# Kernel tuning notes

Measured on AMD Instinct MI355X. Metric: run time of the kernel, lower is better.

Reference implementation:

```python
import jax, jax.numpy as jnp
import numpy as np

B, N, C_IN, C_OUT, BASIS = 8, 128, 64, 64, 15
AVG_NOBJ = 49.0
NEG_SLOPE = 0.01  # torch LeakyReLU default


def eops_2_to_2_sum(x, average_nobj=AVG_NOBJ):
    """x: [B, C, N, N] -> [B, C, 15, N, N].
    5 order-zero ops + 10 sum-aggregation ops (sums normalized by average_nobj,
    double sums by average_nobj**2, as in PELICAN's 'sum' aggregation)."""
    n = x.shape[-1]
    eye = jnp.eye(n, dtype=x.dtype)                       # [N, N]
    d = jnp.diagonal(x, axis1=-2, axis2=-1)               # [B, C, N]
    rowsum = x.sum(-1) / average_nobj                      # [B, C, N]
    colsum = x.sum(-2) / average_nobj                      # [B, C, N]
    trace = d.sum(-1) / average_nobj                       # [B, C]
    allsum = x.sum((-2, -1)) / (average_nobj ** 2)         # [B, C]
    bc = lambda v: jnp.broadcast_to(v, x.shape)
    ops = [
        # --- order zero (no aggregation) ---
        d[..., :, None] * eye,                 # diag(A) embedded on diagonal
        bc(d[..., :, None]),                   # A_ii broadcast along j
        bc(d[..., None, :]),                   # A_jj broadcast along i
        x,                                     # identity
        jnp.swapaxes(x, -1, -2),               # transpose
        # --- aggregation ops ---
        rowsum[..., :, None] * eye,            # row sums on diagonal
        colsum[..., :, None] * eye,            # col sums on diagonal
        trace[..., None, None] * eye,          # trace on diagonal
        allsum[..., None, None] * eye,         # total sum on diagonal
        bc(rowsum[..., :, None]),              # rowsum_i broadcast along j
        bc(rowsum[..., None, :]),              # rowsum_j broadcast along i
        bc(colsum[..., :, None]),              # colsum_i broadcast along j
        bc(colsum[..., None, :]),              # colsum_j broadcast along i
        bc(trace[..., None, None]),            # trace broadcast everywhere
        bc(allsum[..., None, None]),           # total sum broadcast everywhere
    ]
    return jnp.stack(ops, axis=2)              # [B, C, 15, N, N]


def setup_inputs() -> dict:
    key = jax.random.key(0)
    ks = jax.random.split(key, 5)
    inputs = jax.random.normal(ks[0], (B, N, N, C_IN), jnp.float32)
    mask = jnp.ones((B, N, N, 1), jnp.float32)
    nobj = jnp.full((B,), float(N), jnp.float32)
    s_b = float(np.sqrt(1.0 / BASIS))
    s_d = float(np.sqrt(1.0 / C_IN))
    coefs00 = jax.random.normal(ks[1], (C_IN, BASIS), jnp.float32) * s_b
    coefs01 = jax.random.normal(ks[2], (C_OUT, BASIS), jnp.float32) * s_b
    coefs10 = jax.random.normal(ks[3], (C_IN, C_OUT), jnp.float32) * s_d
    coefs11 = jax.random.normal(ks[4], (C_IN, C_OUT), jnp.float32) * s_d
    bias = jnp.zeros((C_OUT,), jnp.float32)
    diag_bias = jnp.zeros((C_OUT,), jnp.float32)
    return {"inputs": inputs, "mask": mask, "nobj": nobj,
            "coefs00": coefs00, "coefs01": coefs01,
            "coefs10": coefs10, "coefs11": coefs11,
            "bias": bias, "diag_bias": diag_bias}


def reference(inputs, mask, nobj, coefs00, coefs01, coefs10, coefs11, bias, diag_bias):
    # inputs: [B, N, N, C_in] -> channels-first for basis construction
    x = jnp.transpose(inputs, (0, 3, 1, 2))                     # [B, C, N, N]
    ops = eops_2_to_2_sum(x)                                    # [B, C, 15, N, N]
    # low-rank reconstructed coefficient tensor [C_in, C_out, 15]
    coefs = (coefs00[:, None, :] * coefs10[:, :, None]
             + coefs01[None, :, :] * coefs11[:, :, None])
    out = jnp.einsum('dsb,ndbij->nijs', coefs, ops)             # [B, N, N, C_out]
    eye = jnp.eye(inputs.shape[1], dtype=out.dtype)[None, :, :, None]
    out = out + bias[None, None, None, :] + eye * diag_bias[None, None, None, :]
    out = jax.nn.leaky_relu(out, NEG_SLOPE)
    return out * mask
```

## Files before the change

### kernel.cpp

```cpp
#include <hip/hip_runtime.h>

#define BB 8
#define NN 128
#define CC 64
static constexpr float INV_A = 1.0f / 49.0f;

#define OFF_C    0
#define OFF_CB   61440
#define OFF_RS   65536
#define OFF_CS   131072
#define OFF_DV   196608
#define OFF_TR   262144
#define OFF_AS   262656
#define OFF_U1   263168
#define OFF_U2   328704
#define OFF_DG   394240

typedef __attribute__((ext_vector_type(8))) short v8s;
typedef __attribute__((ext_vector_type(4))) float v4f;

static __device__ inline unsigned pack2bf(float a, float b) {
    union { float f; unsigned u; } ua, ub; ua.f = a; ub.f = b;
    return ((ua.u + 0x8000u) >> 16) | ((ub.u + 0x8000u) & 0xffff0000u);
}
static __device__ inline unsigned short f2bf(float a) {
    union { float f; unsigned u; } ua; ua.f = a;
    return (unsigned short)((ua.u + 0x8000u) >> 16);
}

__global__ void k_coefs(const float* __restrict__ c00, const float* __restrict__ c01,
                        const float* __restrict__ c10, const float* __restrict__ c11,
                        float* __restrict__ ws) {
    int idx = blockIdx.x * 256 + threadIdx.x;
    if (idx < 15 * 4096) {
        int b = idx >> 12; int r = idx & 4095; int d = r >> 6; int s = r & 63;
        ws[OFF_C + idx] = c00[d * 15 + b] * c10[d * 64 + s] + c01[s * 15 + b] * c11[d * 64 + s];
    } else if (idx < 15 * 4096 + 8192) {
        int k = idx - 15 * 4096;
        int which = k >> 12;
        int r = k & 4095; int s = r >> 6; int d = r & 63;
        int b = 3 + which;
        float v = c00[d * 15 + b] * c10[d * 64 + s] + c01[s * 15 + b] * c11[d * 64 + s];
        unsigned short* cb = (unsigned short*)(ws + OFF_CB);
        cb[s * 128 + which * 64 + d] = f2bf(v);
    }
}

__global__ void k_reduce(const float* __restrict__ in, float* __restrict__ ws) {
    __shared__ float4 part[4][4][16];
    int mode = blockIdx.x >> 8;
    int bb = blockIdx.x & 255;
    int n = bb >> 5; int g0 = (bb & 31) * 4;
    int t = threadIdx.x;
    int q = t >> 6; int ii = (t >> 4) & 3; int d4 = t & 15;
    float4 acc = make_float4(0.f, 0.f, 0.f, 0.f);
    if (mode == 0) {
        int i = g0 + ii;
        float4 dvv = acc; bool hd = false;
        const float* base = in + ((size_t)(n * NN + i)) * NN * CC + d4 * 4;
        for (int j = q * 32; j < q * 32 + 32; ++j) {
            float4 v = *(const float4*)(base + (size_t)j * CC);
            acc.x += v.x; acc.y += v.y; acc.z += v.z; acc.w += v.w;
            if (j == i) { dvv = v; hd = true; }
        }
        if (hd) *(float4*)(ws + OFF_DV + ((size_t)(n * NN + i)) * CC + d4 * 4) = dvv;
    } else {
        int j = g0 + ii;
        for (int i = q * 32; i < q * 32 + 32; ++i) {
            float4 v = *(const float4*)(in + (((size_t)(n * NN + i)) * NN + j) * CC + d4 * 4);
            acc.x += v.x; acc.y += v.y; acc.z += v.z; acc.w += v.w;
        }
    }
    part[q][ii][d4] = acc;
    __syncthreads();
    if (t < 64) {
        int i2 = t >> 4; int dd = t & 15;
        float4 a = part[0][i2][dd], b = part[1][i2][dd], c = part[2][i2][dd], d = part[3][i2][dd];
        float4 s;
        s.x = (a.x + b.x + c.x + d.x) * INV_A;
        s.y = (a.y + b.y + c.y + d.y) * INV_A;
        s.z = (a.z + b.z + c.z + d.z) * INV_A;
        s.w = (a.w + b.w + c.w + d.w) * INV_A;
        *(float4*)(ws + (mode ? OFF_CS : OFF_RS) + ((size_t)(n * NN + g0 + i2)) * CC + dd * 4) = s;
    }
}

__global__ void k_traces(float* __restrict__ ws) {
    __shared__ float pt[4][64], pa[4][64];
    int n = blockIdx.x; int t = threadIdx.x;
    int d = t & 63; int q = t >> 6;
    float tr = 0.f, as = 0.f;
    for (int e = 0; e < 32; ++e) {
        int i = q * 32 + e;
        tr += ws[OFF_DV + ((size_t)(n * NN + i)) * CC + d];
        as += ws[OFF_RS + ((size_t)(n * NN + i)) * CC + d];
    }
    pt[q][d] = tr; pa[q][d] = as;
    __syncthreads();
    if (t < 64) {
        float T = pt[0][t] + pt[1][t] + pt[2][t] + pt[3][t];
        float A2 = pa[0][t] + pa[1][t] + pa[2][t] + pa[3][t];
        ws[OFF_TR + n * CC + t] = T * INV_A;
        ws[OFF_AS + n * CC + t] = A2 * INV_A;
    }
}

__global__ void k_uv(const float* __restrict__ bias, const float* __restrict__ dbias,
                     float* __restrict__ ws) {
    int n = blockIdx.x >> 5; int i0 = (blockIdx.x & 31) * 4; int s = threadIdx.x;
    const float* C = ws + OFF_C;
    float aU1[4] = {0, 0, 0, 0}, aU2[4] = {0, 0, 0, 0}, aDG[4] = {0, 0, 0, 0};
    float aS = 0.f, aDGc = 0.f;
    for (int dc = 0; dc < 16; ++dc) {
        float tr4[4], as4[4], dv4[4][4], rs4[4][4], cs4[4][4];
        {
            float4 v = *(const float4*)(ws + OFF_TR + n * CC + dc * 4);
            tr4[0] = v.x; tr4[1] = v.y; tr4[2] = v.z; tr4[3] = v.w;
            float4 w = *(const float4*)(ws + OFF_AS + n * CC + dc * 4);
            as4[0] = w.x; as4[1] = w.y; as4[2] = w.z; as4[3] = w.w;
        }
        #pragma unroll
        for (int ii = 0; ii < 4; ++ii) {
            size_t ro = ((size_t)(n * NN + i0 + ii)) * CC + dc * 4;
            float4 v = *(const float4*)(ws + OFF_DV + ro);
            dv4[ii][0] = v.x; dv4[ii][1] = v.y; dv4[ii][2] = v.z; dv4[ii][3] = v.w;
            float4 r = *(const float4*)(ws + OFF_RS + ro);
            rs4[ii][0] = r.x; rs4[ii][1] = r.y; rs4[ii][2] = r.z; rs4[ii][3] = r.w;
            float4 c = *(const float4*)(ws + OFF_CS + ro);
            cs4[ii][0] = c.x; cs4[ii][1] = c.y; cs4[ii][2] = c.z; cs4[ii][3] = c.w;
        }
        #pragma unroll
        for (int k = 0; k < 4; ++k) {
            int d = dc * 4 + k;
            const float* Cd = C + d * 64 + s;
            float c0 = Cd[0 * 4096], c1 = Cd[1 * 4096], c2 = Cd[2 * 4096];
            float c5 = Cd[5 * 4096], c6 = Cd[6 * 4096], c7 = Cd[7 * 4096];
            float c8 = Cd[8 * 4096], c9 = Cd[9 * 4096], c10v = Cd[10 * 4096];
            float c11v = Cd[11 * 4096], c12v = Cd[12 * 4096];
            float c13 = Cd[13 * 4096], c14 = Cd[14 * 4096];
            aS += c13 * tr4[k] + c14 * as4[k];
            aDGc += c7 * tr4[k] + c8 * as4[k];
            #pragma unroll
            for (int ii = 0; ii < 4; ++ii) {
                aU1[ii] += c1 * dv4[ii][k] + c9 * rs4[ii][k] + c11v * cs4[ii][k];
                aU2[ii] += c2 * dv4[ii][k] + c10v * rs4[ii][k] + c12v * cs4[ii][k];
                aDG[ii] += c0 * dv4[ii][k] + c5 * rs4[ii][k] + c6 * cs4[ii][k];
            }
        }
    }
    float bs = bias[s], dbs = dbias[s];
    for (int ii = 0; ii < 4; ++ii) {
        size_t row = ((size_t)(n * NN + i0 + ii)) * CC + s;
        ws[OFF_U1 + row] = aU1[ii] + aS + bs;
        ws[OFF_U2 + row] = aU2[ii];
        ws[OFF_DG + row] = aDG[ii] + aDGc + dbs;
    }
}

__global__ __launch_bounds__(256, 4) void k_main(
        const float* __restrict__ in, const float* __restrict__ mask,
        const float* __restrict__ ws, float* __restrict__ out) {
    __shared__ __align__(16) unsigned char smem[34816 + 17408];
    unsigned short* Ab = (unsigned short*)smem;
    unsigned short* Bb = (unsigned short*)(smem + 17408);
    float* Obuf = (float*)smem;

    int blk = blockIdx.x;
    int n = blk >> 8; int rem = blk & 255; int i = rem >> 1; int j0 = (rem & 1) * 64;
    int t = threadIdx.x;
    int tp = t >> 4; int c = t & 15;

    const unsigned short* cb = (const unsigned short*)(ws + OFF_CB);
    {
        int cc8 = t & 15;
        #pragma unroll
        for (int e = 0; e < 4; ++e) {
            int s = e * 16 + tp;
            float4 v = *(const float4*)(cb + s * 128 + cc8 * 8);
            *(float4*)((unsigned char*)(Bb + s * 136 + cc8 * 8)) = v;
        }
    }
    {
        const float* src = in + (((size_t)(n * NN + i)) * NN + j0) * CC;
        #pragma unroll
        for (int e = 0; e < 4; ++e) {
            int p = e * 16 + tp;
            float4 v = *(const float4*)(src + (size_t)p * CC + c * 4);
            uint2 pk; pk.x = pack2bf(v.x, v.y); pk.y = pack2bf(v.z, v.w);
            *(uint2*)(Ab + p * 136 + c * 4) = pk;
        }
    }
    {
        #pragma unroll
        for (int e = 0; e < 4; ++e) {
            int p = e * 16 + tp;
            const float* src = in + (((size_t)(n * NN + (j0 + p))) * NN + i) * CC;
            float4 v = *(const float4*)(src + c * 4);
            uint2 pk; pk.x = pack2bf(v.x, v.y); pk.y = pack2bf(v.z, v.w);
            *(uint2*)(Ab + p * 136 + 64 + c * 4) = pk;
        }
    }
    __syncthreads();

    int w = t >> 6; int l = t & 63;
    int r16 = l & 15; int quad = l >> 4;
    v4f acc[4];
    #pragma unroll
    for (int st = 0; st < 4; ++st) acc[st] = 0.f;
    int arow = w * 16 + r16;
    #pragma unroll
    for (int kk = 0; kk < 4; ++kk) {
        v8s af = *(const v8s*)(Ab + arow * 136 + kk * 32 + quad * 8);
        #pragma unroll
        for (int st = 0; st < 4; ++st) {
            v8s bfr = *(const v8s*)(Bb + (st * 16 + r16) * 136 + kk * 32 + quad * 8);
            acc[st] = __builtin_amdgcn_mfma_f32_16x16x32_bf16(af, bfr, acc[st], 0, 0, 0);
        }
    }
    #pragma unroll
    for (int st = 0; st < 4; ++st)
        #pragma unroll
        for (int reg = 0; reg < 4; ++reg)
            Obuf[(w * 16 + quad * 4 + reg) * 68 + st * 16 + r16] = acc[st][reg];
    __syncthreads();

    int srow = (n * NN + i) * CC;
    float4 u1 = *(const float4*)(ws + OFF_U1 + srow + c * 4);
    float4 dg = *(const float4*)(ws + OFF_DG + srow + c * 4);
    #pragma unroll
    for (int e = 0; e < 4; ++e) {
        int p = e * 16 + tp;
        int j = j0 + p;
        float4 v = *(const float4*)(Obuf + p * 68 + c * 4);
        float4 u2 = *(const float4*)(ws + OFF_U2 + (n * NN + j) * CC + c * 4);
        v.x += u1.x + u2.x; v.y += u1.y + u2.y; v.z += u1.z + u2.z; v.w += u1.w + u2.w;
        if (j == i) { v.x += dg.x; v.y += dg.y; v.z += dg.z; v.w += dg.w; }
        v.x = v.x > 0.f ? v.x : 0.01f * v.x;
        v.y = v.y > 0.f ? v.y : 0.01f * v.y;
        v.z = v.z > 0.f ? v.z : 0.01f * v.z;
        v.w = v.w > 0.f ? v.w : 0.01f * v.w;
        float m = mask[((size_t)(n * NN + i)) * NN + j];
        v.x *= m; v.y *= m; v.z *= m; v.w *= m;
        *(float4*)(out + (((size_t)(n * NN + i)) * NN + j) * CC + c * 4) = v;
    }
}

extern "C" void kernel_launch(void* const* d_in, const int* in_sizes, int n_in,
                              void* d_out, int out_size, void* d_ws, size_t ws_size,
                              hipStream_t stream) {
    const float* inputs = (const float*)d_in[0];
    const float* mask   = (const float*)d_in[1];
    const float* c00 = (const float*)d_in[3];
    const float* c01 = (const float*)d_in[4];
    const float* c10 = (const float*)d_in[5];
    const float* c11 = (const float*)d_in[6];
    const float* bias  = (const float*)d_in[7];
    const float* dbias = (const float*)d_in[8];
    float* out = (float*)d_out;
    float* ws = (float*)d_ws;

    k_coefs <<<272, 256, 0, stream>>>(c00, c01, c10, c11, ws);
    k_reduce<<<512, 256, 0, stream>>>(inputs, ws);
    k_traces<<<8, 256, 0, stream>>>(ws);
    k_uv    <<<256, 64, 0, stream>>>(bias, dbias, ws);
    k_main  <<<2048, 256, 0, stream>>>(inputs, mask, ws, out);
}
```

Measured before the change: 151.0 us.

## Merge preprocessing kernels and split k_uv channel reduction across four waves

Folds the coefficient-building kernel into the reduction kernel as extra blocks, and folds the trace/allsum computation into k_uv, so five launches become three. k_uv now runs 256 threads per block, each wave covering a quarter of the input channels, with partial sums combined through shared memory. This is meant to cut launch overhead and the long serial channel loop in the low-occupancy k_uv. The cost is that every k_uv block recomputes the per-batch traces, and the extra shared memory and barriers add some overhead. k_main's shared buffer is also trimmed to the size it actually uses, which may allow more resident blocks.

```diff
diff --git a/kernel.cpp b/kernel.cpp
--- a/kernel.cpp
+++ b/kernel.cpp
@@ -10,8 +10,6 @@
 #define OFF_RS   65536
 #define OFF_CS   131072
 #define OFF_DV   196608
-#define OFF_TR   262144
-#define OFF_AS   262656
 #define OFF_U1   263168
 #define OFF_U2   328704
 #define OFF_DG   394240
@@ -28,25 +26,26 @@
     return (unsigned short)((ua.u + 0x8000u) >> 16);
 }
 
-__global__ void k_coefs(const float* __restrict__ c00, const float* __restrict__ c01,
-                        const float* __restrict__ c10, const float* __restrict__ c11,
-                        float* __restrict__ ws) {
-    int idx = blockIdx.x * 256 + threadIdx.x;
-    if (idx < 15 * 4096) {
-        int b = idx >> 12; int r = idx & 4095; int d = r >> 6; int s = r & 63;
-        ws[OFF_C + idx] = c00[d * 15 + b] * c10[d * 64 + s] + c01[s * 15 + b] * c11[d * 64 + s];
-    } else if (idx < 15 * 4096 + 8192) {
-        int k = idx - 15 * 4096;
-        int which = k >> 12;
-        int r = k & 4095; int s = r >> 6; int d = r & 63;
-        int b = 3 + which;
-        float v = c00[d * 15 + b] * c10[d * 64 + s] + c01[s * 15 + b] * c11[d * 64 + s];
-        unsigned short* cb = (unsigned short*)(ws + OFF_CB);
-        cb[s * 128 + which * 64 + d] = f2bf(v);
-    }
-}
-
-__global__ void k_reduce(const float* __restrict__ in, float* __restrict__ ws) {
+__global__ void k_pre(const float* __restrict__ in,
+                      const float* __restrict__ c00, const float* __restrict__ c01,
+                      const float* __restrict__ c10, const float* __restrict__ c11,
+                      float* __restrict__ ws) {
+    if (blockIdx.x >= 512) {
+        int idx = (blockIdx.x - 512) * 256 + threadIdx.x;
+        if (idx < 15 * 4096) {
+            int b = idx >> 12; int r = idx & 4095; int d = r >> 6; int s = r & 63;
+            ws[OFF_C + idx] = c00[d * 15 + b] * c10[d * 64 + s] + c01[s * 15 + b] * c11[d * 64 + s];
+        } else if (idx < 15 * 4096 + 8192) {
+            int k = idx - 15 * 4096;
+            int which = k >> 12;
+            int r = k & 4095; int s = r >> 6; int d = r & 63;
+            int b = 3 + which;
+            float v = c00[d * 15 + b] * c10[d * 64 + s] + c01[s * 15 + b] * c11[d * 64 + s];
+            unsigned short* cb = (unsigned short*)(ws + OFF_CB);
+            cb[s * 128 + which * 64 + d] = f2bf(v);
+        }
+        return;
+    }
     __shared__ float4 part[4][4][16];
     int mode = blockIdx.x >> 8;
     int bb = blockIdx.x & 255;
@@ -85,40 +84,42 @@
     }
 }
 
-__global__ void k_traces(float* __restrict__ ws) {
-    __shared__ float pt[4][64], pa[4][64];
-    int n = blockIdx.x; int t = threadIdx.x;
-    int d = t & 63; int q = t >> 6;
-    float tr = 0.f, as = 0.f;
-    for (int e = 0; e < 32; ++e) {
-        int i = q * 32 + e;
-        tr += ws[OFF_DV + ((size_t)(n * NN + i)) * CC + d];
-        as += ws[OFF_RS + ((size_t)(n * NN + i)) * CC + d];
-    }
-    pt[q][d] = tr; pa[q][d] = as;
-    __syncthreads();
-    if (t < 64) {
-        float T = pt[0][t] + pt[1][t] + pt[2][t] + pt[3][t];
-        float A2 = pa[0][t] + pa[1][t] + pa[2][t] + pa[3][t];
-        ws[OFF_TR + n * CC + t] = T * INV_A;
-        ws[OFF_AS + n * CC + t] = A2 * INV_A;
-    }
-}
-
-__global__ void k_uv(const float* __restrict__ bias, const float* __restrict__ dbias,
-                     float* __restrict__ ws) {
-    int n = blockIdx.x >> 5; int i0 = (blockIdx.x & 31) * 4; int s = threadIdx.x;
+__global__ __launch_bounds__(256, 4) void k_uv(const float* __restrict__ bias,
+                                               const float* __restrict__ dbias,
+                                               float* __restrict__ ws) {
+    __shared__ float trL[64], asL[64];
+    __shared__ float pU1[4][4][64], pU2[4][4][64], pDG[4][4][64];
+    __shared__ float pS[4][64], pDGc[4][64];
+    int n = blockIdx.x >> 5; int i0 = (blockIdx.x & 31) * 4;
+    int t = threadIdx.x;
+    int s = t & 63; int q = t >> 6;
+
+    {
+        float tr = 0.f, as = 0.f;
+        #pragma unroll 4
+        for (int e = 0; e < 32; ++e) {
+            int i = q * 32 + e;
+            tr += ws[OFF_DV + ((size_t)(n * NN + i)) * CC + s];
+            as += ws[OFF_RS + ((size_t)(n * NN + i)) * CC + s];
+        }
+        pS[q][s] = tr; pDGc[q][s] = as;
+        __syncthreads();
+        if (t < 64) {
+            trL[t] = (pS[0][t] + pS[1][t] + pS[2][t] + pS[3][t]) * INV_A;
+            asL[t] = (pDGc[0][t] + pDGc[1][t] + pDGc[2][t] + pDGc[3][t]) * INV_A;
+        }
+        __syncthreads();
+    }
+
     const float* C = ws + OFF_C;
     float aU1[4] = {0, 0, 0, 0}, aU2[4] = {0, 0, 0, 0}, aDG[4] = {0, 0, 0, 0};
     float aS = 0.f, aDGc = 0.f;
-    for (int dc = 0; dc < 16; ++dc) {
+    #pragma unroll
+    for (int c4 = 0; c4 < 4; ++c4) {
+        int dc = q * 4 + c4;
         float tr4[4], as4[4], dv4[4][4], rs4[4][4], cs4[4][4];
-        {
-            float4 v = *(const float4*)(ws + OFF_TR + n * CC + dc * 4);
-            tr4[0] = v.x; tr4[1] = v.y; tr4[2] = v.z; tr4[3] = v.w;
-            float4 w = *(const float4*)(ws + OFF_AS + n * CC + dc * 4);
-            as4[0] = w.x; as4[1] = w.y; as4[2] = w.z; as4[3] = w.w;
-        }
+        #pragma unroll
+        for (int k = 0; k < 4; ++k) { tr4[k] = trL[dc * 4 + k]; as4[k] = asL[dc * 4 + k]; }
         #pragma unroll
         for (int ii = 0; ii < 4; ++ii) {
             size_t ro = ((size_t)(n * NN + i0 + ii)) * CC + dc * 4;
@@ -148,19 +149,29 @@
             }
         }
     }
-    float bs = bias[s], dbs = dbias[s];
+    #pragma unroll
     for (int ii = 0; ii < 4; ++ii) {
-        size_t row = ((size_t)(n * NN + i0 + ii)) * CC + s;
-        ws[OFF_U1 + row] = aU1[ii] + aS + bs;
-        ws[OFF_U2 + row] = aU2[ii];
-        ws[OFF_DG + row] = aDG[ii] + aDGc + dbs;
-    }
+        pU1[q][ii][s] = aU1[ii]; pU2[q][ii][s] = aU2[ii]; pDG[q][ii][s] = aDG[ii];
+    }
+    pS[q][s] = aS; pDGc[q][s] = aDGc;
+    __syncthreads();
+
+    int fi = q;
+    float u1 = pU1[0][fi][s] + pU1[1][fi][s] + pU1[2][fi][s] + pU1[3][fi][s];
+    float u2 = pU2[0][fi][s] + pU2[1][fi][s] + pU2[2][fi][s] + pU2[3][fi][s];
+    float dg = pDG[0][fi][s] + pDG[1][fi][s] + pDG[2][fi][s] + pDG[3][fi][s];
+    float aSt = pS[0][s] + pS[1][s] + pS[2][s] + pS[3][s];
+    float aDGct = pDGc[0][s] + pDGc[1][s] + pDGc[2][s] + pDGc[3][s];
+    size_t row = ((size_t)(n * NN + i0 + fi)) * CC + s;
+    ws[OFF_U1 + row] = u1 + aSt + bias[s];
+    ws[OFF_U2 + row] = u2;
+    ws[OFF_DG + row] = dg + aDGct + dbias[s];
 }
 
 __global__ __launch_bounds__(256, 4) void k_main(
         const float* __restrict__ in, const float* __restrict__ mask,
         const float* __restrict__ ws, float* __restrict__ out) {
-    __shared__ __align__(16) unsigned char smem[34816 + 17408];
+    __shared__ __align__(16) unsigned char smem[34816];
     unsigned short* Ab = (unsigned short*)smem;
     unsigned short* Bb = (unsigned short*)(smem + 17408);
     float* Obuf = (float*)smem;
@@ -171,14 +182,11 @@
     int tp = t >> 4; int c = t & 15;
 
     const unsigned short* cb = (const unsigned short*)(ws + OFF_CB);
-    {
-        int cc8 = t & 15;
-        #pragma unroll
-        for (int e = 0; e < 4; ++e) {
-            int s = e * 16 + tp;
-            float4 v = *(const float4*)(cb + s * 128 + cc8 * 8);
-            *(float4*)((unsigned char*)(Bb + s * 136 + cc8 * 8)) = v;
-        }
+    #pragma unroll
+    for (int e = 0; e < 4; ++e) {
+        int s = e * 16 + tp;
+        float4 v = *(const float4*)(cb + s * 128 + c * 8);
+        *(float4*)((unsigned char*)(Bb + s * 136 + c * 8)) = v;
     }
     {
         const float* src = in + (((size_t)(n * NN + i)) * NN + j0) * CC;
@@ -190,15 +198,13 @@
             *(uint2*)(Ab + p * 136 + c * 4) = pk;
         }
     }
-    {
-        #pragma unroll
-        for (int e = 0; e < 4; ++e) {
-            int p = e * 16 + tp;
-            const float* src = in + (((size_t)(n * NN + (j0 + p))) * NN + i) * CC;
-            float4 v = *(const float4*)(src + c * 4);
-            uint2 pk; pk.x = pack2bf(v.x, v.y); pk.y = pack2bf(v.z, v.w);
-            *(uint2*)(Ab + p * 136 + 64 + c * 4) = pk;
-        }
+    #pragma unroll
+    for (int e = 0; e < 4; ++e) {
+        int p = e * 16 + tp;
+        const float* src = in + (((size_t)(n * NN + (j0 + p))) * NN + i) * CC;
+        float4 v = *(const float4*)(src + c * 4);
+        uint2 pk; pk.x = pack2bf(v.x, v.y); pk.y = pack2bf(v.z, v.w);
+        *(uint2*)(Ab + p * 136 + 64 + c * 4) = pk;
     }
     __syncthreads();
 
@@ -259,9 +265,7 @@
     float* out = (float*)d_out;
     float* ws = (float*)d_ws;
 
-    k_coefs <<<272, 256, 0, stream>>>(c00, c01, c10, c11, ws);
-    k_reduce<<<512, 256, 0, stream>>>(inputs, ws);
-    k_traces<<<8, 256, 0, stream>>>(ws);
-    k_uv    <<<256, 64, 0, stream>>>(bias, dbias, ws);
-    k_main  <<<2048, 256, 0, stream>>>(inputs, mask, ws, out);
-}
+    k_pre <<<784, 256, 0, stream>>>(inputs, c00, c01, c10, c11, ws);
+    k_uv  <<<256, 256, 0, stream>>>(bias, dbias, ws);
+    k_main<<<2048, 256, 0, stream>>>(inputs, mask, ws, out);
+}
```

Result: faster. 136.9 us (-9.4%).
